# Optimization experiments

Measured on AMD Instinct MI355X. Metric: run time of the kernel, lower is better.

Reference implementation:

```python
import jax, jax.numpy as jnp
import numpy as np

NH, NP, HD = 8, 4, 32  # num_heads, num_points, head_dim (C=256)


def setup_inputs() -> dict:
    key = jax.random.key(0)
    k = jax.random.split(key, 8)
    B, Nq, H, W, C = 4, 8192, 128, 128, 256
    query = jax.random.normal(k[0], (B, Nq, C), jnp.float32)
    reference_points = jax.random.uniform(k[1], (B, Nq, 2), jnp.float32)
    value = jax.random.normal(k[2], (B, H * W, C), jnp.float32)
    s = 1.0 / np.sqrt(C).astype(np.float32)
    W_off = jax.random.normal(k[3], (C, NH * NP * 2), jnp.float32) * s
    b_off = jax.random.normal(k[4], (NH * NP * 2,), jnp.float32) * 0.5
    W_attn = jax.random.normal(k[5], (C, NH * NP), jnp.float32) * s
    b_attn = jnp.zeros((NH * NP,), jnp.float32)
    W_val = jax.random.normal(k[6], (C, C), jnp.float32) * s
    b_val = jnp.zeros((C,), jnp.float32)
    W_out = jax.random.normal(k[7], (C, C), jnp.float32) * s
    b_out = jnp.zeros((C,), jnp.float32)
    return dict(query=query, reference_points=reference_points, value=value,
                W_off=W_off, b_off=b_off, W_attn=W_attn, b_attn=b_attn,
                W_val=W_val, b_val=b_val, W_out=W_out, b_out=b_out, Hs=H, Ws=W)


def reference(query, reference_points, value, W_off, b_off, W_attn, b_attn,
              W_val, b_val, W_out, b_out, Hs, Ws):
    B, Nq, C = query.shape
    # sampling offsets and attention weights from queries
    off = (query @ W_off + b_off).reshape(B, Nq, NH, NP, 2)
    attn = jax.nn.softmax((query @ W_attn + b_attn).reshape(B, Nq, NH, NP), axis=-1)
    off = jnp.stack([off[..., 0] / Ws * 0.1, off[..., 1] / Hs * 0.1], axis=-1)
    loc = jnp.clip(reference_points[:, :, None, None, :] + off, 0.0, 1.0)  # [B,Nq,NH,NP,2] (x,y)
    # project value and arrange per head: [B, NH, H*W, HD]
    v = (value @ W_val + b_val).reshape(B, Hs, Ws, NH, HD)
    v = v.transpose(0, 3, 1, 2, 4).reshape(B, NH, Hs * Ws, HD)
    # grid_sample bilinear, align_corners=False, padding_mode='border':
    # pixel coord = loc*size - 0.5, clamped to [0, size-1]
    gx = jnp.clip(loc[..., 0] * Ws - 0.5, 0.0, Ws - 1.0)
    gy = jnp.clip(loc[..., 1] * Hs - 0.5, 0.0, Hs - 1.0)
    x0 = jnp.floor(gx); y0 = jnp.floor(gy)
    fx = gx - x0; fy = gy - y0
    x0i = x0.astype(jnp.int32); y0i = y0.astype(jnp.int32)
    x1i = jnp.minimum(x0i + 1, Ws - 1); y1i = jnp.minimum(y0i + 1, Hs - 1)

    def flat(xi, yi):  # [B,Nq,NH,NP] -> [B,NH,Nq*NP]
        return (yi * Ws + xi).transpose(0, 2, 1, 3).reshape(B, NH, Nq * NP)

    def gather(idx):  # -> [B,NH,Nq*NP,HD]
        return jnp.take_along_axis(v, idx[..., None], axis=2)

    def wts(w):  # [B,Nq,NH,NP] -> [B,NH,Nq*NP,1]
        return w.transpose(0, 2, 1, 3).reshape(B, NH, Nq * NP, 1)

    samp = (wts((1 - fx) * (1 - fy)) * gather(flat(x0i, y0i))
            + wts(fx * (1 - fy)) * gather(flat(x1i, y0i))
            + wts((1 - fx) * fy) * gather(flat(x0i, y1i))
            + wts(fx * fy) * gather(flat(x1i, y1i)))
    samp = samp.reshape(B, NH, Nq, NP, HD)
    aw = attn.transpose(0, 2, 1, 3)[..., None]  # [B,NH,Nq,NP,1]
    out = (samp * aw).sum(axis=3)               # [B,NH,Nq,HD]
    out = out.transpose(0, 2, 1, 3).reshape(B, Nq, C)
    return out @ W_out + b_out
```

## Files before the change

### kernel.cpp

```cpp
#include <hip/hip_runtime.h>
#include <cstddef>

#define B_   4
#define NQ_  8192
#define C_   256
#define H_   128
#define W_   128
#define HW_  (H_ * W_)
#define NH_  8
#define NP_  4
#define HD_  32

typedef __attribute__((ext_vector_type(8))) short s16x8;
typedef __attribute__((ext_vector_type(4))) float f32x4;

__device__ __forceinline__ short f2bf(float x) {
    unsigned u = __float_as_uint(x);
    unsigned r = (u + 0x7FFFu + ((u >> 16) & 1u)) >> 16;
    return (short)r;
}
__device__ __forceinline__ void gload_lds16(const void* g, void* l) {
    __builtin_amdgcn_global_load_lds(
        (const __attribute__((address_space(1))) void*)g,
        (__attribute__((address_space(3))) void*)l, 16, 0, 0);
}

__global__ void prep_kernel(const float* __restrict__ Wv, const float* __restrict__ Wo,
                            const float* __restrict__ Woff, const float* __restrict__ Wattn,
                            const float* __restrict__ boff, const float* __restrict__ battn,
                            short* __restrict__ BtVal, short* __restrict__ BtOut,
                            short* __restrict__ BtOA, float* __restrict__ biasOA)
{
    const int b = blockIdx.x, t = threadIdx.x;
    if (b < 256) {
        const int n = b;
        BtVal[(size_t)n * 256 + t] = f2bf(Wv[(size_t)t * 256 + n]);
    } else if (b < 512) {
        const int n = b - 256;
        BtOut[(size_t)n * 256 + t] = f2bf(Wo[(size_t)t * 256 + n]);
    } else {
        const int n = b - 512;
        float v = (n < 64) ? Woff[(size_t)t * 64 + n]
                           : (n < 96 ? Wattn[(size_t)t * 32 + (n - 64)] : 0.f);
        BtOA[(size_t)n * 256 + t] = f2bf(v);
        if (t == 0) biasOA[n] = (n < 64) ? boff[n] : (n < 96 ? battn[n - 64] : 0.f);
    }
}

template<int AMODE>
__device__ __forceinline__ void gemm_body(
    const void* __restrict__ Ap, const short* __restrict__ Bt,
    const float* __restrict__ bias, void* __restrict__ Cp,
    int ldc, int omode, int m0, int n0, short* As, short* Bs)
{
    const int tid = threadIdx.x;
    const int l = tid & 63;
    const int w = tid >> 6;
    const int wm = w >> 1, wn = w & 1;

    f32x4 acc[4][4];
#pragma unroll
    for (int i = 0; i < 4; ++i)
#pragma unroll
        for (int j = 0; j < 4; ++j) acc[i][j] = (f32x4)0.f;

    const int frag_r = l & 15;
    const int kslot  = (l >> 4) * 8;
    const int arow = tid >> 1, ahalf = tid & 1;
    const float* Af = (const float*)Ap;
    const short* A16 = (const short*)Ap;

    float4 fA0, fA1, fA2, fA3;

#define STAGE_B(k0, buf)                                                      \
    _Pragma("unroll")                                                         \
    for (int r = 0; r < 2; ++r) {                                             \
        const int i = r * 256 + tid;                                          \
        gload_lds16(&Bt[(size_t)(n0 + (i >> 2)) * 256 + (k0) + (i & 3) * 8],  \
                    (char*)Bs + (buf) * 8192 + r * 4096 + w * 1024);          \
    }
#define STAGE_A_LDS(k0, buf)                                                  \
    _Pragma("unroll")                                                         \
    for (int r = 0; r < 2; ++r) {                                             \
        const int i = r * 256 + tid;                                          \
        gload_lds16(&A16[(size_t)(m0 + (i >> 2)) * 256 + (k0) + (i & 3) * 8], \
                    (char*)As + (buf) * 8192 + r * 4096 + w * 1024);          \
    }
#define LOAD_A_REGS(k0)                                                       \
    {                                                                         \
        const float* src = &Af[(size_t)(m0 + arow) * 256 + (k0) + ahalf * 16];\
        fA0 = ((const float4*)src)[0];                                        \
        fA1 = ((const float4*)src)[1];                                        \
        fA2 = ((const float4*)src)[2];                                        \
        fA3 = ((const float4*)src)[3];                                        \
    }
#define WRITE_A(buf)                                                          \
    {                                                                         \
        union { short s[8]; s16x8 v; } p0, p1;                                \
        p0.s[0]=f2bf(fA0.x); p0.s[1]=f2bf(fA0.y); p0.s[2]=f2bf(fA0.z); p0.s[3]=f2bf(fA0.w); \
        p0.s[4]=f2bf(fA1.x); p0.s[5]=f2bf(fA1.y); p0.s[6]=f2bf(fA1.z); p0.s[7]=f2bf(fA1.w); \
        p1.s[0]=f2bf(fA2.x); p1.s[1]=f2bf(fA2.y); p1.s[2]=f2bf(fA2.z); p1.s[3]=f2bf(fA2.w); \
        p1.s[4]=f2bf(fA3.x); p1.s[5]=f2bf(fA3.y); p1.s[6]=f2bf(fA3.z); p1.s[7]=f2bf(fA3.w); \
        *(s16x8*)&As[(buf) * 4096 + arow * 32 + ahalf * 16]     = p0.v;       \
        *(s16x8*)&As[(buf) * 4096 + arow * 32 + ahalf * 16 + 8] = p1.v;       \
    }

    STAGE_B(0, 0);
    if (AMODE == 0) { STAGE_A_LDS(0, 0); }
    else            { LOAD_A_REGS(0); WRITE_A(0); }
    __syncthreads();

#pragma unroll
    for (int k = 0; k < 8; ++k) {
        const int cur = k & 1, nxt = cur ^ 1;
        if (k < 7) {
            STAGE_B((k + 1) * 32, nxt);
            if (AMODE == 0) { STAGE_A_LDS((k + 1) * 32, nxt); }
            else            { LOAD_A_REGS((k + 1) * 32); }
        }
        s16x8 a[4], b[4];
#pragma unroll
        for (int mf = 0; mf < 4; ++mf)
            a[mf] = *(const s16x8*)&As[cur * 4096 + (wm * 64 + mf * 16 + frag_r) * 32 + kslot];
#pragma unroll
        for (int nf = 0; nf < 4; ++nf)
            b[nf] = *(const s16x8*)&Bs[cur * 4096 + (wn * 64 + nf * 16 + frag_r) * 32 + kslot];
#pragma unroll
        for (int mf = 0; mf < 4; ++mf)
#pragma unroll
            for (int nf = 0; nf < 4; ++nf)
                acc[mf][nf] = __builtin_amdgcn_mfma_f32_16x16x32_bf16(
                    a[mf], b[nf], acc[mf][nf], 0, 0, 0);
        if (k < 7) {
            if (AMODE == 1) WRITE_A(nxt);
            __syncthreads();
        }
    }
#undef STAGE_B
#undef STAGE_A_LDS
#undef LOAD_A_REGS
#undef WRITE_A

    const int col_local = wn * 64 + (l & 15);
    const int rbase = wm * 64 + (l >> 4) * 4;
    if (omode == 0) {
#pragma unroll
        for (int nf = 0; nf < 4; ++nf) {
            const int n = n0 + col_local + nf * 16;
            const float bs = bias[n];
#pragma unroll
            for (int mf = 0; mf < 4; ++mf) {
                const f32x4 v = acc[mf][nf];
#pragma unroll
                for (int rr = 0; rr < 4; ++rr)
                    ((float*)Cp)[(size_t)(m0 + rbase + mf * 16 + rr) * ldc + n] = v[rr] + bs;
            }
        }
    } else {
#pragma unroll
        for (int nf = 0; nf < 4; ++nf) {
            const int n = n0 + col_local + nf * 16;
            const float bs = bias[n];
            const int h = n >> 5, d = n & 31;
#pragma unroll
            for (int mf = 0; mf < 4; ++mf) {
                const f32x4 v = acc[mf][nf];
#pragma unroll
                for (int rr = 0; rr < 4; ++rr) {
                    const int m = m0 + rbase + mf * 16 + rr;
                    const int bb = m >> 14, pix = m & (HW_ - 1);
                    ((short*)Cp)[((size_t)(bb * NH_ + h) * HW_ + pix) * HD_ + d] = f2bf(v[rr] + bs);
                }
            }
        }
    }
}

__global__ __launch_bounds__(256, 4)
void gemm_k1k2a(const float* __restrict__ value, const short* __restrict__ BtVal,
                const float* __restrict__ b_val, short* __restrict__ vproj,
                const float* __restrict__ query, const short* __restrict__ BtOA,
                const float* __restrict__ biasOA, float* __restrict__ oa)
{
    __shared__ short As[2 * 4096];
    __shared__ short Bs[2 * 4096];
    const int bid = blockIdx.x;
    if (bid < 1024) {
        gemm_body<1>(value, BtVal, b_val, vproj, 0, 2,
                     (bid >> 1) * 128, (bid & 1) * 128, As, Bs);
    } else {
        gemm_body<1>(query, BtOA, biasOA, oa, 128, 0,
                     (bid - 1024) * 128, 0, As, Bs);
    }
}

__global__ __launch_bounds__(256, 4)
void gemm_k3(const short* __restrict__ samp, const short* __restrict__ BtOut,
             const float* __restrict__ b_out, float* __restrict__ out)
{
    __shared__ short As[2 * 4096];
    __shared__ short Bs[2 * 4096];
    gemm_body<0>(samp, BtOut, b_out, out, 256, 0,
                 (blockIdx.x >> 1) * 128, (blockIdx.x & 1) * 128, As, Bs);
}

__global__ __launch_bounds__(256)
void sample_kernel(const float* __restrict__ oa,
                   const float* __restrict__ ref,
                   const short* __restrict__ vproj,
                   short* __restrict__ samp)
{
    __shared__ int4   s_idx[2][32];
    __shared__ float4 s_w[2][32];
    const int tid = threadIdx.x;
    const int q0 = blockIdx.x * 2;

    if (tid < 64) {
        const int qq = tid >> 5;
        const int hp = tid & 31;
        const int h = hp >> 2, p = hp & 3;
        const int q = q0 + qq;
        const float logit = oa[(size_t)q * 128 + 64 + h * 4 + p];
        float mx = fmaxf(logit, __shfl_xor(logit, 1));
        mx = fmaxf(mx, __shfl_xor(mx, 2));
        float e = __expf(logit - mx);
        float s = e + __shfl_xor(e, 1);
        s += __shfl_xor(s, 2);
        const float aw = e / s;

        const float ox = oa[(size_t)q * 128 + h * 8 + p * 2 + 0] * (0.1f / (float)W_);
        const float oy = oa[(size_t)q * 128 + h * 8 + p * 2 + 1] * (0.1f / (float)H_);
        const float lx = fminf(fmaxf(ref[(size_t)q * 2 + 0] + ox, 0.f), 1.f);
        const float ly = fminf(fmaxf(ref[(size_t)q * 2 + 1] + oy, 0.f), 1.f);
        const float gx = fminf(fmaxf(lx * (float)W_ - 0.5f, 0.f), (float)(W_ - 1));
        const float gy = fminf(fmaxf(ly * (float)H_ - 0.5f, 0.f), (float)(H_ - 1));
        const float x0f = floorf(gx), y0f = floorf(gy);
        const float fx = gx - x0f, fy = gy - y0f;
        const int x0 = (int)x0f, y0 = (int)y0f;
        const int x1 = min(x0 + 1, W_ - 1), y1 = min(y0 + 1, H_ - 1);
        s_idx[qq][hp] = make_int4((y0 * W_ + x0) * HD_, (y0 * W_ + x1) * HD_,
                                  (y1 * W_ + x0) * HD_, (y1 * W_ + x1) * HD_);
        const float gx1 = 1.f - fx, gy1 = 1.f - fy;
        s_w[qq][hp] = make_float4(aw * gx1 * gy1, aw * fx * gy1,
                                  aw * gx1 * fy,  aw * fx * fy);
    }
    __syncthreads();

    const int qq = tid >> 7;
    const int t = tid & 127;
    const int h = t >> 4;
    const int d0 = (t & 15) * 2;
    const int q = q0 + qq;
    const int b = q >> 13;
    const short* vh = vproj + (size_t)(b * NH_ + h) * (HW_ * HD_) + d0;

    float a0 = 0.f, a1 = 0.f;
#pragma unroll
    for (int p = 0; p < 4; ++p) {
        const int4   ii = s_idx[qq][h * 4 + p];
        const float4 ww = s_w[qq][h * 4 + p];
        unsigned v;
        v = *(const unsigned*)&vh[ii.x];
        a0 = fmaf(ww.x, __uint_as_float(v << 16), a0);
        a1 = fmaf(ww.x, __uint_as_float(v & 0xFFFF0000u), a1);
        v = *(const unsigned*)&vh[ii.y];
        a0 = fmaf(ww.y, __uint_as_float(v << 16), a0);
        a1 = fmaf(ww.y, __uint_as_float(v & 0xFFFF0000u), a1);
        v = *(const unsigned*)&vh[ii.z];
        a0 = fmaf(ww.z, __uint_as_float(v << 16), a0);
        a1 = fmaf(ww.z, __uint_as_float(v & 0xFFFF0000u), a1);
        v = *(const unsigned*)&vh[ii.w];
        a0 = fmaf(ww.w, __uint_as_float(v << 16), a0);
        a1 = fmaf(ww.w, __uint_as_float(v & 0xFFFF0000u), a1);
    }
    const unsigned lo = (unsigned)(unsigned short)f2bf(a0);
    const unsigned hi = (unsigned)(unsigned short)f2bf(a1);
    ((unsigned*)samp)[((size_t)q * 256 + h * HD_ + d0) >> 1] = lo | (hi << 16);
}

extern "C" void kernel_launch(void* const* d_in, const int* in_sizes, int n_in,
                              void* d_out, int out_size, void* d_ws, size_t ws_size,
                              hipStream_t stream)
{
    const float* query  = (const float*)d_in[0];
    const float* refpt  = (const float*)d_in[1];
    const float* value  = (const float*)d_in[2];
    const float* W_off  = (const float*)d_in[3];
    const float* b_off  = (const float*)d_in[4];
    const float* W_attn = (const float*)d_in[5];
    const float* b_attn = (const float*)d_in[6];
    const float* W_val  = (const float*)d_in[7];
    const float* b_val  = (const float*)d_in[8];
    const float* W_out  = (const float*)d_in[9];
    const float* b_out  = (const float*)d_in[10];
    float* out = (float*)d_out;

    char* ws = (char*)d_ws;
    short* vproj  = (short*)ws;
    short* samp   = (short*)(ws + (size_t)32 * 1024 * 1024);
    float* oa     = (float*)(ws + (size_t)48 * 1024 * 1024);
    short* BtVal  = (short*)(ws + (size_t)64 * 1024 * 1024);
    short* BtOut  = BtVal + 256 * 256;
    short* BtOA   = BtOut + 256 * 256;
    float* biasOA = (float*)(BtOA + 128 * 256);

    prep_kernel<<<640, 256, 0, stream>>>(W_val, W_out, W_off, W_attn,
                                         b_off, b_attn, BtVal, BtOut, BtOA, biasOA);

    gemm_k1k2a<<<1280, 256, 0, stream>>>(value, BtVal, b_val, vproj,
                                         query, BtOA, biasOA, oa);

    sample_kernel<<<(B_ * NQ_) / 2, 256, 0, stream>>>(oa, refpt, vproj, samp);

    gemm_k3<<<512, 256, 0, stream>>>(samp, BtOut, b_out, out);
}
```

Measured before the change: 84.64 us.

## Stage fp32 A tiles directly to LDS and convert to bf16 at fragment load

The fp32 A operand of the value and query projection GEMMs is now copied straight from global memory into LDS with async global_load_lds, using an XOR swizzle, instead of going through registers, being converted and then stored. Conversion to bf16 moves to fragment load time with the packed v_cvt_pk_bf16_f32 instruction. This frees registers and removes the register round-trip between k-steps. In exchange the A LDS buffer doubles, launch bounds drop to 3 waves per SIMD, and every k-step now does twice as many LDS reads for A plus repeated conversions.

```diff
diff --git a/kernel.cpp b/kernel.cpp
--- a/kernel.cpp
+++ b/kernel.cpp
@@ -18,6 +18,11 @@
     unsigned u = __float_as_uint(x);
     unsigned r = (u + 0x7FFFu + ((u >> 16) & 1u)) >> 16;
     return (short)r;
+}
+__device__ __forceinline__ unsigned cvt_pk_bf16(float lo, float hi) {
+    unsigned r;
+    asm("v_cvt_pk_bf16_f32 %0, %1, %2" : "=v"(r) : "v"(lo), "v"(hi));
+    return r;
 }
 __device__ __forceinline__ void gload_lds16(const void* g, void* l) {
     __builtin_amdgcn_global_load_lds(
@@ -47,12 +52,13 @@
     }
 }
 
-template<int AMODE>
+template<int ADT>
 __device__ __forceinline__ void gemm_body(
     const void* __restrict__ Ap, const short* __restrict__ Bt,
     const float* __restrict__ bias, void* __restrict__ Cp,
-    int ldc, int omode, int m0, int n0, short* As, short* Bs)
-{
+    int ldc, int omode, int m0, int n0, char* AsRaw, short* Bs)
+{
+    constexpr int ABYTES = (ADT == 1) ? 16384 : 8192;
     const int tid = threadIdx.x;
     const int l = tid & 63;
     const int w = tid >> 6;
@@ -66,11 +72,8 @@
 
     const int frag_r = l & 15;
     const int kslot  = (l >> 4) * 8;
-    const int arow = tid >> 1, ahalf = tid & 1;
-    const float* Af = (const float*)Ap;
+    const float* Af  = (const float*)Ap;
     const short* A16 = (const short*)Ap;
-
-    float4 fA0, fA1, fA2, fA3;
 
 #define STAGE_B(k0, buf)                                                      \
     _Pragma("unroll")                                                         \
@@ -79,35 +82,27 @@
         gload_lds16(&Bt[(size_t)(n0 + (i >> 2)) * 256 + (k0) + (i & 3) * 8],  \
                     (char*)Bs + (buf) * 8192 + r * 4096 + w * 1024);          \
     }
-#define STAGE_A_LDS(k0, buf)                                                  \
-    _Pragma("unroll")                                                         \
-    for (int r = 0; r < 2; ++r) {                                             \
-        const int i = r * 256 + tid;                                          \
-        gload_lds16(&A16[(size_t)(m0 + (i >> 2)) * 256 + (k0) + (i & 3) * 8], \
-                    (char*)As + (buf) * 8192 + r * 4096 + w * 1024);          \
-    }
-#define LOAD_A_REGS(k0)                                                       \
-    {                                                                         \
-        const float* src = &Af[(size_t)(m0 + arow) * 256 + (k0) + ahalf * 16];\
-        fA0 = ((const float4*)src)[0];                                        \
-        fA1 = ((const float4*)src)[1];                                        \
-        fA2 = ((const float4*)src)[2];                                        \
-        fA3 = ((const float4*)src)[3];                                        \
-    }
-#define WRITE_A(buf)                                                          \
-    {                                                                         \
-        union { short s[8]; s16x8 v; } p0, p1;                                \
-        p0.s[0]=f2bf(fA0.x); p0.s[1]=f2bf(fA0.y); p0.s[2]=f2bf(fA0.z); p0.s[3]=f2bf(fA0.w); \
-        p0.s[4]=f2bf(fA1.x); p0.s[5]=f2bf(fA1.y); p0.s[6]=f2bf(fA1.z); p0.s[7]=f2bf(fA1.w); \
-        p1.s[0]=f2bf(fA2.x); p1.s[1]=f2bf(fA2.y); p1.s[2]=f2bf(fA2.z); p1.s[3]=f2bf(fA2.w); \
-        p1.s[4]=f2bf(fA3.x); p1.s[5]=f2bf(fA3.y); p1.s[6]=f2bf(fA3.z); p1.s[7]=f2bf(fA3.w); \
-        *(s16x8*)&As[(buf) * 4096 + arow * 32 + ahalf * 16]     = p0.v;       \
-        *(s16x8*)&As[(buf) * 4096 + arow * 32 + ahalf * 16 + 8] = p1.v;       \
+#define STAGE_A(k0, buf)                                                      \
+    if (ADT == 0) {                                                           \
+        _Pragma("unroll")                                                     \
+        for (int r = 0; r < 2; ++r) {                                         \
+            const int i = r * 256 + tid;                                      \
+            gload_lds16(&A16[(size_t)(m0 + (i >> 2)) * 256 + (k0) + (i & 3) * 8], \
+                        AsRaw + (buf) * ABYTES + r * 4096 + w * 1024);        \
+        }                                                                     \
+    } else {                                                                  \
+        _Pragma("unroll")                                                     \
+        for (int r = 0; r < 4; ++r) {                                         \
+            const int i = r * 256 + tid;                                      \
+            const int row = i >> 3, s = i & 7;                                \
+            const int colf = (s * 4) ^ ((row & 7) << 2);      \
+            gload_lds16(&Af[(size_t)(m0 + row) * 256 + (k0) + colf],          \
+                        AsRaw + (buf) * ABYTES + r * 4096 + w * 1024);        \
+        }                                                                     \
     }
 
     STAGE_B(0, 0);
-    if (AMODE == 0) { STAGE_A_LDS(0, 0); }
-    else            { LOAD_A_REGS(0); WRITE_A(0); }
+    STAGE_A(0, 0);
     __syncthreads();
 
 #pragma unroll
@@ -115,13 +110,27 @@
         const int cur = k & 1, nxt = cur ^ 1;
         if (k < 7) {
             STAGE_B((k + 1) * 32, nxt);
-            if (AMODE == 0) { STAGE_A_LDS((k + 1) * 32, nxt); }
-            else            { LOAD_A_REGS((k + 1) * 32); }
+            STAGE_A((k + 1) * 32, nxt);
         }
         s16x8 a[4], b[4];
 #pragma unroll
-        for (int mf = 0; mf < 4; ++mf)
-            a[mf] = *(const s16x8*)&As[cur * 4096 + (wm * 64 + mf * 16 + frag_r) * 32 + kslot];
+        for (int mf = 0; mf < 4; ++mf) {
+            const int row = wm * 64 + mf * 16 + frag_r;
+            if (ADT == 0) {
+                a[mf] = *(const s16x8*)(AsRaw + cur * ABYTES + row * 64 + kslot * 2);
+            } else {
+                const int g0 = (l >> 4) * 2;
+                const char* base = AsRaw + cur * ABYTES + row * 128;
+                const float4 q0 = *(const float4*)(base + ((g0 * 16)       ^ ((row & 7) << 4)));
+                const float4 q1 = *(const float4*)(base + (((g0 + 1) * 16) ^ ((row & 7) << 4)));
+                union { unsigned u[4]; s16x8 v; } pk;
+                pk.u[0] = cvt_pk_bf16(q0.x, q0.y);
+                pk.u[1] = cvt_pk_bf16(q0.z, q0.w);
+                pk.u[2] = cvt_pk_bf16(q1.x, q1.y);
+                pk.u[3] = cvt_pk_bf16(q1.z, q1.w);
+                a[mf] = pk.v;
+            }
+        }
 #pragma unroll
         for (int nf = 0; nf < 4; ++nf)
             b[nf] = *(const s16x8*)&Bs[cur * 4096 + (wn * 64 + nf * 16 + frag_r) * 32 + kslot];
@@ -131,15 +140,10 @@
             for (int nf = 0; nf < 4; ++nf)
                 acc[mf][nf] = __builtin_amdgcn_mfma_f32_16x16x32_bf16(
                     a[mf], b[nf], acc[mf][nf], 0, 0, 0);
-        if (k < 7) {
-            if (AMODE == 1) WRITE_A(nxt);
-            __syncthreads();
-        }
+        if (k < 7) __syncthreads();
     }
 #undef STAGE_B
-#undef STAGE_A_LDS
-#undef LOAD_A_REGS
-#undef WRITE_A
+#undef STAGE_A
 
     const int col_local = wn * 64 + (l & 15);
     const int rbase = wm * 64 + (l >> 4) * 4;
@@ -176,21 +180,21 @@
     }
 }
 
-__global__ __launch_bounds__(256, 4)
+__global__ __launch_bounds__(256, 3)
 void gemm_k1k2a(const float* __restrict__ value, const short* __restrict__ BtVal,
                 const float* __restrict__ b_val, short* __restrict__ vproj,
                 const float* __restrict__ query, const short* __restrict__ BtOA,
                 const float* __restrict__ biasOA, float* __restrict__ oa)
 {
-    __shared__ short As[2 * 4096];
+    __shared__ char  AsRaw[2 * 16384];
     __shared__ short Bs[2 * 4096];
     const int bid = blockIdx.x;
     if (bid < 1024) {
         gemm_body<1>(value, BtVal, b_val, vproj, 0, 2,
-                     (bid >> 1) * 128, (bid & 1) * 128, As, Bs);
+                     (bid >> 1) * 128, (bid & 1) * 128, AsRaw, Bs);
     } else {
         gemm_body<1>(query, BtOA, biasOA, oa, 128, 0,
-                     (bid - 1024) * 128, 0, As, Bs);
+                     (bid - 1024) * 128, 0, AsRaw, Bs);
     }
 }
 
@@ -198,10 +202,10 @@
 void gemm_k3(const short* __restrict__ samp, const short* __restrict__ BtOut,
              const float* __restrict__ b_out, float* __restrict__ out)
 {
-    __shared__ short As[2 * 4096];
+    __shared__ char  AsRaw[2 * 8192];
     __shared__ short Bs[2 * 4096];
     gemm_body<0>(samp, BtOut, b_out, out, 256, 0,
-                 (blockIdx.x >> 1) * 128, (blockIdx.x & 1) * 128, As, Bs);
+                 (blockIdx.x >> 1) * 128, (blockIdx.x & 1) * 128, AsRaw, Bs);
 }
 
 __global__ __launch_bounds__(256)
```

Measured after the change: 79.84 us. -5.7%, faster.
